# Performance work log

Measured on AMD Instinct MI355X. Metric: run time of the kernel, lower is better.

The kernel has to match this reference:

```python
import jax, jax.numpy as jnp
import numpy as np

N_GRIDS = 16
N_FEATS = 2
GRID_SHAPE = (64, 64, 64)  # D, H, W
NODES = 64
N_OUT = 1
DATA_MIN = 0.0
DATA_MAX = 1.0
N_POINTS = 524288


def setup_inputs() -> dict:
    key = jax.random.key(0)
    ks = jax.random.split(key, 12)
    x = jax.random.uniform(ks[0], (N_POINTS, 3), jnp.float32, -1.0, 1.0)
    # matches randomize_grids(): scales ~ log(1 - U*0.05), rotations ~ identity quat + noise,
    # translations ~ U(-0.05, 0.05)
    scales = jnp.log(1.0 - jax.random.uniform(ks[1], (N_GRIDS, 3), jnp.float32) * 0.05)
    rotations = jnp.zeros((N_GRIDS, 4), jnp.float32).at[:, 3].set(1.0) \
        + jax.random.normal(ks[2], (N_GRIDS, 4), jnp.float32) * 0.05
    translations = jax.random.uniform(ks[3], (N_GRIDS, 3), jnp.float32) * 0.1 - 0.05
    # original uses U(-1e-4, 1e-4); use a larger scale for numerically meaningful outputs
    feature_grids = jax.random.uniform(ks[4], (N_GRIDS, N_FEATS) + GRID_SHAPE,
                                       jnp.float32, -0.1, 0.1)
    d_in = N_GRIDS * N_FEATS
    def xavier(k, fi, fo):
        std = np.sqrt(2.0 / (fi + fo)).astype(np.float32)
        return jax.random.normal(k, (fi, fo), jnp.float32) * std
    W0 = xavier(ks[5], d_in, NODES)
    b0 = jax.random.normal(ks[6], (NODES,), jnp.float32) * 0.001
    W1 = xavier(ks[7], NODES, NODES)
    b1 = jax.random.normal(ks[8], (NODES,), jnp.float32) * 0.001
    W2 = xavier(ks[9], NODES, N_OUT)
    b2 = jax.random.normal(ks[10], (N_OUT,), jnp.float32) * 0.001
    return {"x": x, "rotations": rotations, "scales": scales,
            "translations": translations, "feature_grids": feature_grids,
            "W0": W0, "b0": b0, "W1": W1, "b1": b1, "W2": W2, "b2": b2}


def quat_to_rot(q):
    # q: [G,4] in (x, y, z, w) order; normalized (rotation_activation)
    q = q / jnp.linalg.norm(q, axis=-1, keepdims=True)
    x, y, z, w = q[:, 0], q[:, 1], q[:, 2], q[:, 3]
    r0 = jnp.stack([1 - 2 * (y * y + z * z), 2 * (x * y - z * w), 2 * (x * z + y * w)], -1)
    r1 = jnp.stack([2 * (x * y + z * w), 1 - 2 * (x * x + z * z), 2 * (y * z - x * w)], -1)
    r2 = jnp.stack([2 * (x * z - y * w), 2 * (y * z + x * w), 1 - 2 * (x * x + y * y)], -1)
    return jnp.stack([r0, r1, r2], axis=-2)  # [G,3,3]


def transform_points(x, rotations, scales, translations):
    # S*R*T order: local = diag(exp(scales)) @ R @ x + t, per grid -> [G,N,3]
    R = quat_to_rot(rotations)
    s = jnp.exp(scales)
    M = s[:, :, None] * R  # [G,3,3]
    return jnp.einsum('gij,nj->gni', M, x) + translations[:, None, :]


def trilinear_sample(grid, pts):
    # grid: [C,D,H,W]; pts: [N,3] (x,y,z) in [-1,1]; grid_sample semantics:
    # mode='bilinear', align_corners=True, padding_mode='zeros'
    C, D, H, W = grid.shape
    fx = (pts[:, 0] + 1.0) * 0.5 * (W - 1)
    fy = (pts[:, 1] + 1.0) * 0.5 * (H - 1)
    fz = (pts[:, 2] + 1.0) * 0.5 * (D - 1)
    x0 = jnp.floor(fx); y0 = jnp.floor(fy); z0 = jnp.floor(fz)
    wx = fx - x0; wy = fy - y0; wz = fz - z0
    x0i = x0.astype(jnp.int32); y0i = y0.astype(jnp.int32); z0i = z0.astype(jnp.int32)

    def corner(dx, dy, dz):
        xi = x0i + dx; yi = y0i + dy; zi = z0i + dz
        valid = (xi >= 0) & (xi < W) & (yi >= 0) & (yi < H) & (zi >= 0) & (zi < D)
        v = grid[:, jnp.clip(zi, 0, D - 1), jnp.clip(yi, 0, H - 1), jnp.clip(xi, 0, W - 1)]
        w = ((wx if dx else 1 - wx) * (wy if dy else 1 - wy) * (wz if dz else 1 - wz))
        return v * jnp.where(valid, w, 0.0)[None, :]

    out = corner(0, 0, 0)
    for dz in (0, 1):
        for dy in (0, 1):
            for dx in (0, 1):
                if (dx, dy, dz) != (0, 0, 0):
                    out = out + corner(dx, dy, dz)
    return out  # [C,N]


def reference(x, rotations, scales, translations, feature_grids, W0, b0, W1, b1, W2, b2):
    pts = transform_points(x, rotations, scales, translations)      # [G,N,3]
    feats = jax.vmap(trilinear_sample)(feature_grids, pts)          # [G,C,N]
    feats = feats.transpose(2, 0, 1).reshape(x.shape[0], -1)        # [N, G*C]
    h = jax.nn.relu(feats @ W0 + b0)
    h = jax.nn.relu(h @ W1 + b1)
    y = h @ W2 + b2
    return y * (DATA_MAX - DATA_MIN) + DATA_MIN
```

## Files before the change

### kernel.cpp

```cpp
#include <hip/hip_runtime.h>
#include <cstddef>
#include <cstdint>

constexpr int NPTS   = 524288;
constexpr int NG     = 16;
constexpr int GR     = 64;
constexpr int GR3    = GR * GR * GR;
constexpr int NNODES = 64;
constexpr int NBINS  = 32768;

constexpr size_t GRIDS_BYTES = (size_t)NG * GR3 * 8;
constexpr size_t WS_SORT     = GRIDS_BYTES;
constexpr size_t SORT_BYTES  = (size_t)NPTS * 16;
constexpr size_t WS_KEYR     = WS_SORT + SORT_BYTES;
constexpr size_t KEYR_BYTES  = (size_t)NPTS * 4;
constexpr size_t WS_BINS     = WS_KEYR + KEYR_BYTES;
constexpr size_t BINS_BYTES  = (size_t)NBINS * 4;
constexpr size_t WS_MATS     = WS_BINS + BINS_BYTES;
constexpr size_t MATS_BYTES  = 1024;
constexpr size_t WS_WPACK    = WS_MATS + MATS_BYTES;
constexpr size_t WPACK_BYTES = (size_t)(256 + 512) * 16;
constexpr size_t WS_PART     = WS_WPACK + WPACK_BYTES;
constexpr size_t PART_BYTES  = 128 * 4;
constexpr size_t WS_TOTAL    = WS_PART + PART_BYTES;

constexpr int PREP_REPACK = 4096;
constexpr int PREP_HIST   = 2048;

typedef _Float16 half8 __attribute__((ext_vector_type(8)));
typedef float    floatx4 __attribute__((ext_vector_type(4)));

__device__ __forceinline__ unsigned part1by2(unsigned x) {
    x &= 0x3ff;
    x = (x | (x << 16)) & 0x030000FF;
    x = (x | (x <<  8)) & 0x0300F00F;
    x = (x | (x <<  4)) & 0x030C30C3;
    x = (x | (x <<  2)) & 0x09249249;
    return x;
}

__device__ __forceinline__ unsigned cell_of(float px, float py, float pz) {
    int cx = (int)((px + 1.0f) * 16.0f); cx = min(max(cx, 0), 31);
    int cy = (int)((py + 1.0f) * 16.0f); cy = min(max(cy, 0), 31);
    int cz = (int)((pz + 1.0f) * 16.0f); cz = min(max(cz, 0), 31);
    return part1by2((unsigned)cx) | (part1by2((unsigned)cy) << 1) | (part1by2((unsigned)cz) << 2);
}

__device__ __forceinline__ unsigned f32_to_bf16_rne(float f) {
    unsigned u = __float_as_uint(f);
    return (u + 0x7fffu + ((u >> 16) & 1u)) >> 16;
}

__device__ __forceinline__ unsigned pack_h2(float a, float b) {
    unsigned short ua = __builtin_bit_cast(unsigned short, (_Float16)a);
    unsigned short ub = __builtin_bit_cast(unsigned short, (_Float16)b);
    return (unsigned)ua | ((unsigned)ub << 16);
}

__device__ __forceinline__ unsigned short f32_to_h16(float a) {
    return __builtin_bit_cast(unsigned short, (_Float16)a);
}

__global__ __launch_bounds__(256) void prep_kernel(
    const float* __restrict__ grids, uint2* __restrict__ gout,
    const float* __restrict__ xs, unsigned* __restrict__ bins,
    unsigned* __restrict__ keyrank,
    const float* __restrict__ rot, const float* __restrict__ scl,
    const float* __restrict__ trn, float* __restrict__ mats,
    const float* __restrict__ W0, const float* __restrict__ W1,
    uint4* __restrict__ wpack)
{
    const int bid = blockIdx.x;
    const int tid = threadIdx.x;

    if (bid < PREP_REPACK) {
        const int base = (bid * 256 + tid) * 4;
        const int g    = base >> 18;
        const int node = base & (GR3 - 1);
        const int x    = node & 63;
        const float* p0 = grids + (size_t)g * 2 * GR3 + node;
        const float* p1 = p0 + GR3;
        const float4 c0 = *(const float4*)p0;
        const float4 c1 = *(const float4*)p1;
        float d0n, d1n;
        if (x == 60) { d0n = c0.w; d1n = c1.w; }
        else         { d0n = p0[4]; d1n = p1[4]; }
        const float e0[5] = {c0.x, c0.y, c0.z, c0.w, d0n};
        const float e1[5] = {c1.x, c1.y, c1.z, c1.w, d1n};
        unsigned pk[5];
        #pragma unroll
        for (int i = 0; i < 5; ++i)
            pk[i] = f32_to_bf16_rne(e0[i]) | (f32_to_bf16_rne(e1[i]) << 16);
        uint4* dst = (uint4*)(gout + (size_t)g * GR3 + node);
        dst[0] = make_uint4(pk[0], pk[1], pk[1], pk[2]);
        dst[1] = make_uint4(pk[2], pk[3], pk[3], pk[4]);
    } else if (bid < PREP_REPACK + PREP_HIST) {
        const int n = (bid - PREP_REPACK) * 256 + tid;
        const unsigned key = cell_of(xs[n*3+0], xs[n*3+1], xs[n*3+2]);
        const unsigned rank = atomicAdd(&bins[key], 1u);
        keyrank[n] = key | (rank << 15);
    } else if (bid == PREP_REPACK + PREP_HIST) {
        const int g = tid;
        if (g < NG) {
            float qx = rot[g*4+0], qy = rot[g*4+1], qz = rot[g*4+2], qw = rot[g*4+3];
            const float inv = 1.0f / sqrtf(qx*qx + qy*qy + qz*qz + qw*qw);
            qx *= inv; qy *= inv; qz *= inv; qw *= inv;
            const float sx = expf(scl[g*3+0]);
            const float sy = expf(scl[g*3+1]);
            const float sz = expf(scl[g*3+2]);
            float* m = mats + g * 12;
            m[0] = sx * (1.0f - 2.0f*(qy*qy + qz*qz));
            m[1] = sx * (2.0f*(qx*qy - qz*qw));
            m[2] = sx * (2.0f*(qx*qz + qy*qw));
            m[3] = sy * (2.0f*(qx*qy + qz*qw));
            m[4] = sy * (1.0f - 2.0f*(qx*qx + qz*qz));
            m[5] = sy * (2.0f*(qy*qz - qx*qw));
            m[6] = sz * (2.0f*(qx*qz - qy*qw));
            m[7] = sz * (2.0f*(qy*qz + qx*qw));
            m[8] = sz * (1.0f - 2.0f*(qx*qx + qy*qy));
            m[9]  = trn[g*3+0];
            m[10] = trn[g*3+1];
            m[11] = trn[g*3+2];
        }
    } else {
        const int t = tid >> 6;
        const int lane = tid & 63;
        const int q = lane >> 4, c = lane & 15;
        const int n = t * 16 + c;
        {
            unsigned u[4];
            #pragma unroll
            for (int jj = 0; jj < 4; ++jj) {
                const int k0 = q * 8 + 2 * jj;
                u[jj] = pack_h2(W0[k0 * NNODES + n], W0[(k0 + 1) * NNODES + n]);
            }
            wpack[t * 64 + lane] = make_uint4(u[0], u[1], u[2], u[3]);
        }
        #pragma unroll
        for (int ks = 0; ks < 2; ++ks) {
            unsigned u[4];
            #pragma unroll
            for (int jj = 0; jj < 4; ++jj) {
                const int k0 = ks * 32 + q * 8 + 2 * jj;
                u[jj] = pack_h2(W1[k0 * NNODES + n], W1[(k0 + 1) * NNODES + n]);
            }
            wpack[256 + (ks * 4 + t) * 64 + lane] = make_uint4(u[0], u[1], u[2], u[3]);
        }
    }
}

__global__ __launch_bounds__(256) void scanA_kernel(unsigned* __restrict__ bins,
                                                    unsigned* __restrict__ part) {
    __shared__ unsigned s[256];
    const int t = threadIdx.x;
    const int base = blockIdx.x * 256;
    const unsigned v = bins[base + t];
    s[t] = v;
    __syncthreads();
    for (int off = 1; off < 256; off <<= 1) {
        unsigned u = (t >= off) ? s[t - off] : 0u;
        __syncthreads();
        s[t] += u;
        __syncthreads();
    }
    bins[base + t] = s[t] - v;
    if (t == 255) part[blockIdx.x] = s[255];
}

__global__ __launch_bounds__(128) void scanB_kernel(unsigned* __restrict__ part) {
    __shared__ unsigned s[128];
    const int t = threadIdx.x;
    const unsigned v = part[t];
    s[t] = v;
    __syncthreads();
    for (int off = 1; off < 128; off <<= 1) {
        unsigned u = (t >= off) ? s[t - off] : 0u;
        __syncthreads();
        s[t] += u;
        __syncthreads();
    }
    part[t] = s[t] - v;
}

__global__ __launch_bounds__(256) void scatter_kernel(const float* __restrict__ xs,
                                                      const unsigned* __restrict__ bins,
                                                      const unsigned* __restrict__ part,
                                                      const unsigned* __restrict__ keyrank,
                                                      float4* __restrict__ sorted) {
    const int n = blockIdx.x * 256 + threadIdx.x;
    if (n >= NPTS) return;
    const unsigned kr = keyrank[n];
    const unsigned key = kr & 0x7fffu;
    const unsigned rank = kr >> 15;
    const unsigned pos = part[key >> 8] + bins[key] + rank;
    sorted[pos] = make_float4(xs[n*3+0], xs[n*3+1], xs[n*3+2], __int_as_float(n));
}

struct Geom {
    unsigned i00, i01, i10, i11;
    float ax0, ax1, ay0, ay1, az0, az1;
};

__device__ __forceinline__ Geom make_geom(const float* __restrict__ m,
                                          float px, float py, float pz, int g) {
    Geom G;
    const float tx = fmaf(m[0], px, fmaf(m[1], py, fmaf(m[2], pz, m[9])));
    const float ty = fmaf(m[3], px, fmaf(m[4], py, fmaf(m[5], pz, m[10])));
    const float tz = fmaf(m[6], px, fmaf(m[7], py, fmaf(m[8], pz, m[11])));
    const float fx = (tx + 1.0f) * 31.5f;
    const float fy = (ty + 1.0f) * 31.5f;
    const float fz = (tz + 1.0f) * 31.5f;
    const float x0f = floorf(fx), y0f = floorf(fy), z0f = floorf(fz);
    const float wx = fx - x0f, wy = fy - y0f, wz = fz - z0f;
    const int x0 = (int)x0f, y0 = (int)y0f, z0 = (int)z0f;
    float ax0 = ((unsigned)x0       < 64u) ? (1.0f - wx) : 0.0f;
    float ax1 = ((unsigned)(x0 + 1) < 64u) ? wx          : 0.0f;
    const bool wrap = (x0 == -1);
    G.ax0 = wrap ? ax1 : ax0;
    G.ax1 = wrap ? 0.0f : ax1;
    G.ay0 = ((unsigned)y0       < 64u) ? (1.0f - wy) : 0.0f;
    G.ay1 = ((unsigned)(y0 + 1) < 64u) ? wy          : 0.0f;
    G.az0 = ((unsigned)z0       < 64u) ? (1.0f - wz) : 0.0f;
    G.az1 = ((unsigned)(z0 + 1) < 64u) ? wz          : 0.0f;
    const int xb  = min(max(x0, 0), 63);
    const int yc0 = min(max(y0, 0), 63),     yc1 = min(max(y0 + 1, 0), 63);
    const int zc0 = min(max(z0, 0), 63),     zc1 = min(max(z0 + 1, 0), 63);
    const unsigned b = (unsigned)(g << 18) + (unsigned)xb;
    G.i00 = b + (unsigned)((zc0 << 12) + (yc0 << 6));
    G.i01 = b + (unsigned)((zc0 << 12) + (yc1 << 6));
    G.i10 = b + (unsigned)((zc1 << 12) + (yc0 << 6));
    G.i11 = b + (unsigned)((zc1 << 12) + (yc1 << 6));
    return G;
}

__device__ __forceinline__ void acc_pair(float& f0, float& f1, const Geom& G,
                                         uint2 q, float wyz) {
    float s0 = G.ax0 * __uint_as_float(q.x << 16);
    s0 = fmaf(G.ax1, __uint_as_float(q.y << 16), s0);
    f0 = fmaf(wyz, s0, f0);
    float s1 = G.ax0 * __uint_as_float(q.x & 0xffff0000u);
    s1 = fmaf(G.ax1, __uint_as_float(q.y & 0xffff0000u), s1);
    f1 = fmaf(wyz, s1, f1);
}

constexpr int ARENA_H = 64 * 64;

__device__ __forceinline__ int sw_addr(int row, int halfcol) {
    return row * 64 + ((((halfcol >> 3) ^ (row & 7)) << 3) | (halfcol & 7));
}

__global__ __launch_bounds__(256, 4) void amgsrn_main(
    const float4* __restrict__ sorted,
    const uint2*  __restrict__ gridsP,
    const float*  __restrict__ mats,
    const uint4*  __restrict__ wpack,
    const float*  __restrict__ b0,
    const float*  __restrict__ b1,
    const float*  __restrict__ W2,
    const float*  __restrict__ b2,
    float* __restrict__ out)
{
    __shared__ unsigned short sh[4 * ARENA_H];

    const int tid  = threadIdx.x;
    const int lane = tid & 63;
    const int wv   = tid >> 6;
    const int c    = lane & 15;
    const int q    = lane >> 4;
    unsigned short* wa = sh + wv * ARENA_H;

    const int n = blockIdx.x * 256 + tid;
    const float4 p = sorted[n];
    const float px = p.x, py = p.y, pz = p.z;
    const int orig = __float_as_int(p.w);

    unsigned pk[NG];
    Geom Ga = make_geom(mats, px, py, pz, 0);
    uint2 a00 = gridsP[Ga.i00], a01 = gridsP[Ga.i01];
    uint2 a10 = gridsP[Ga.i10], a11 = gridsP[Ga.i11];
    Geom Gb = make_geom(mats + 12, px, py, pz, 1);
    uint2 b00 = gridsP[Gb.i00], b01 = gridsP[Gb.i01];
    uint2 b10 = gridsP[Gb.i10], b11 = gridsP[Gb.i11];
    #pragma unroll
    for (int g = 0; g < NG; ++g) {
        Geom Gn;
        uint2 n00, n01, n10, n11;
        if (g + 2 < NG) {
            Gn = make_geom(mats + (g + 2) * 12, px, py, pz, g + 2);
            n00 = gridsP[Gn.i00]; n01 = gridsP[Gn.i01];
            n10 = gridsP[Gn.i10]; n11 = gridsP[Gn.i11];
        }
        float f0 = 0.0f, f1 = 0.0f;
        acc_pair(f0, f1, Ga, a00, Ga.az0 * Ga.ay0);
        acc_pair(f0, f1, Ga, a01, Ga.az0 * Ga.ay1);
        acc_pair(f0, f1, Ga, a10, Ga.az1 * Ga.ay0);
        acc_pair(f0, f1, Ga, a11, Ga.az1 * Ga.ay1);
        pk[g] = pack_h2(f0, f1);
        Ga = Gb; a00 = b00; a01 = b01; a10 = b10; a11 = b11;
        if (g + 2 < NG) {
            Gb = Gn; b00 = n00; b01 = n01; b10 = n10; b11 = n11;
        }
    }

    #pragma unroll
    for (int g4 = 0; g4 < 4; ++g4)
        *(uint4*)(wa + sw_addr(lane, g4 * 8)) =
            make_uint4(pk[g4*4+0], pk[g4*4+1], pk[g4*4+2], pk[g4*4+3]);
    __syncthreads();

    half8 a0[4];
    #pragma unroll
    for (int m = 0; m < 4; ++m)
        a0[m] = *(const half8*)(wa + sw_addr(m * 16 + c, q * 8));

    half8 b0f[4], b1f[2][4];
    #pragma unroll
    for (int t = 0; t < 4; ++t)
        b0f[t] = __builtin_bit_cast(half8, wpack[t * 64 + lane]);
    #pragma unroll
    for (int ks = 0; ks < 2; ++ks)
        #pragma unroll
        for (int t = 0; t < 4; ++t)
            b1f[ks][t] = __builtin_bit_cast(half8, wpack[256 + (ks * 4 + t) * 64 + lane]);
    float b0v[4], b1v[4], w2v[4];
    #pragma unroll
    for (int t = 0; t < 4; ++t) {
        b0v[t] = b0[t * 16 + c];
        b1v[t] = b1[t * 16 + c];
        w2v[t] = W2[t * 16 + c];
    }
    const float b2s = b2[0];

    __syncthreads();

    #pragma unroll
    for (int t = 0; t < 4; ++t) {
        #pragma unroll
        for (int m = 0; m < 4; ++m) {
            floatx4 acc = {b0v[t], b0v[t], b0v[t], b0v[t]};
            acc = __builtin_amdgcn_mfma_f32_16x16x32_f16(a0[m], b0f[t], acc, 0, 0, 0);
            const int node = t * 16 + c;
            const int ptb  = m * 16 + q * 4;
            #pragma unroll
            for (int r = 0; r < 4; ++r)
                wa[sw_addr(ptb + r, node)] = f32_to_h16(fmaxf(acc[r], 0.0f));
        }
    }
    __syncthreads();

    half8 a1[4][2];
    #pragma unroll
    for (int m = 0; m < 4; ++m)
        #pragma unroll
        for (int ks = 0; ks < 2; ++ks)
            a1[m][ks] = *(const half8*)(wa + sw_addr(m * 16 + c, ks * 32 + q * 8));

    float p4[4][4];
    #pragma unroll
    for (int m = 0; m < 4; ++m)
        #pragma unroll
        for (int r = 0; r < 4; ++r) p4[m][r] = 0.0f;

    #pragma unroll
    for (int t = 0; t < 4; ++t) {
        #pragma unroll
        for (int m = 0; m < 4; ++m) {
            floatx4 acc = {b1v[t], b1v[t], b1v[t], b1v[t]};
            acc = __builtin_amdgcn_mfma_f32_16x16x32_f16(a1[m][0], b1f[0][t], acc, 0, 0, 0);
            acc = __builtin_amdgcn_mfma_f32_16x16x32_f16(a1[m][1], b1f[1][t], acc, 0, 0, 0);
            #pragma unroll
            for (int r = 0; r < 4; ++r)
                p4[m][r] = fmaf(fmaxf(acc[r], 0.0f), w2v[t], p4[m][r]);
        }
    }

    #pragma unroll
    for (int m = 0; m < 4; ++m)
        #pragma unroll
        for (int r = 0; r < 4; ++r) {
            float v = p4[m][r];
            v += __shfl_xor(v, 1, 64);
            v += __shfl_xor(v, 2, 64);
            v += __shfl_xor(v, 4, 64);
            v += __shfl_xor(v, 8, 64);
            p4[m][r] = v + b2s;
        }

    #pragma unroll
    for (int m = 0; m < 4; ++m)
        #pragma unroll
        for (int r = 0; r < 4; ++r) {
            const int srcPt = m * 16 + q * 4 + r;
            const int origPt = __shfl(orig, srcPt, 64);
            if (c == 0) out[origPt] = p4[m][r];
        }
}

__global__ __launch_bounds__(256, 3) void amgsrn_fused_fallback(
    const float* __restrict__ xs,
    const float* __restrict__ rot,
    const float* __restrict__ scl,
    const float* __restrict__ trn,
    const float* __restrict__ grids,
    const float* __restrict__ W0,
    const float* __restrict__ b0,
    const float* __restrict__ W1,
    const float* __restrict__ b1,
    const float* __restrict__ W2,
    const float* __restrict__ b2,
    float* __restrict__ out)
{
    __shared__ float sM[NG][12];
    const int tid = threadIdx.x;
    if (tid < NG) {
        const int g = tid;
        float qx = rot[g*4+0], qy = rot[g*4+1], qz = rot[g*4+2], qw = rot[g*4+3];
        const float inv = 1.0f / sqrtf(qx*qx + qy*qy + qz*qz + qw*qw);
        qx *= inv; qy *= inv; qz *= inv; qw *= inv;
        const float sx = expf(scl[g*3+0]);
        const float sy = expf(scl[g*3+1]);
        const float sz = expf(scl[g*3+2]);
        sM[g][0] = sx * (1.0f - 2.0f*(qy*qy + qz*qz));
        sM[g][1] = sx * (2.0f*(qx*qy - qz*qw));
        sM[g][2] = sx * (2.0f*(qx*qz + qy*qw));
        sM[g][3] = sy * (2.0f*(qx*qy + qz*qw));
        sM[g][4] = sy * (1.0f - 2.0f*(qx*qx + qz*qz));
        sM[g][5] = sy * (2.0f*(qy*qz - qx*qw));
        sM[g][6] = sz * (2.0f*(qx*qz - qy*qw));
        sM[g][7] = sz * (2.0f*(qy*qz + qx*qw));
        sM[g][8] = sz * (1.0f - 2.0f*(qx*qx + qy*qy));
        sM[g][9]  = trn[g*3+0];
        sM[g][10] = trn[g*3+1];
        sM[g][11] = trn[g*3+2];
    }
    __syncthreads();

    const int n = blockIdx.x * blockDim.x + tid;
    if (n >= NPTS) return;
    const float px = xs[n*3+0];
    const float py = xs[n*3+1];
    const float pz = xs[n*3+2];

    float h0[NNODES];
    #pragma unroll
    for (int j = 0; j < NNODES; ++j) h0[j] = b0[j];

    #pragma unroll
    for (int g = 0; g < NG; ++g) {
        const float* m = sM[g];
        const float tx = m[0]*px + m[1]*py + m[2]*pz + m[9];
        const float ty = m[3]*px + m[4]*py + m[5]*pz + m[10];
        const float tz = m[6]*px + m[7]*py + m[8]*pz + m[11];
        const float fx = (tx + 1.0f) * 31.5f;
        const float fy = (ty + 1.0f) * 31.5f;
        const float fz = (tz + 1.0f) * 31.5f;
        const float x0f = floorf(fx), y0f = floorf(fy), z0f = floorf(fz);
        const float wx = fx - x0f, wy = fy - y0f, wz = fz - z0f;
        const int x0 = (int)x0f, y0 = (int)y0f, z0 = (int)z0f;
        const float* gb = grids + (size_t)g * (size_t)(2 * GR3);
        float f0 = 0.0f, f1 = 0.0f;
        #pragma unroll
        for (int dz = 0; dz < 2; ++dz) {
            #pragma unroll
            for (int dy = 0; dy < 2; ++dy) {
                #pragma unroll
                for (int dx = 0; dx < 2; ++dx) {
                    const int xi = x0 + dx, yi = y0 + dy, zi = z0 + dz;
                    const bool valid = ((unsigned)xi < (unsigned)GR) &
                                       ((unsigned)yi < (unsigned)GR) &
                                       ((unsigned)zi < (unsigned)GR);
                    const int xc = min(max(xi, 0), GR-1);
                    const int yc = min(max(yi, 0), GR-1);
                    const int zc = min(max(zi, 0), GR-1);
                    float w = (dx ? wx : 1.0f - wx) *
                              (dy ? wy : 1.0f - wy) *
                              (dz ? wz : 1.0f - wz);
                    w = valid ? w : 0.0f;
                    const int idx = (zc * GR + yc) * GR + xc;
                    f0 = fmaf(w, gb[idx], f0);
                    f1 = fmaf(w, gb[idx + GR3], f1);
                }
            }
        }
        const float* w0a = W0 + (2*g    ) * NNODES;
        const float* w0b = W0 + (2*g + 1) * NNODES;
        #pragma unroll
        for (int j = 0; j < NNODES; ++j)
            h0[j] = fmaf(f1, w0b[j], fmaf(f0, w0a[j], h0[j]));
    }
    #pragma unroll
    for (int j = 0; j < NNODES; ++j) h0[j] = fmaxf(h0[j], 0.0f);

    float y = b2[0];
    #pragma unroll
    for (int half = 0; half < 2; ++half) {
        float h1[32];
        #pragma unroll
        for (int j = 0; j < 32; ++j) h1[j] = b1[half * 32 + j];
        #pragma unroll
        for (int k = 0; k < NNODES; ++k) {
            const float a = h0[k];
            const float* w = W1 + k * NNODES + half * 32;
            #pragma unroll
            for (int j = 0; j < 32; ++j) h1[j] = fmaf(a, w[j], h1[j]);
        }
        #pragma unroll
        for (int j = 0; j < 32; ++j) y = fmaf(fmaxf(h1[j], 0.0f), W2[half * 32 + j], y);
    }

    out[n] = y;
}

extern "C" void kernel_launch(void* const* d_in, const int* in_sizes, int n_in,
                              void* d_out, int out_size, void* d_ws, size_t ws_size,
                              hipStream_t stream) {
    const float* xs  = (const float*)d_in[0];
    const float* rot = (const float*)d_in[1];
    const float* scl = (const float*)d_in[2];
    const float* trn = (const float*)d_in[3];
    const float* gr  = (const float*)d_in[4];
    const float* W0  = (const float*)d_in[5];
    const float* b0  = (const float*)d_in[6];
    const float* W1  = (const float*)d_in[7];
    const float* b1  = (const float*)d_in[8];
    const float* W2  = (const float*)d_in[9];
    const float* b2  = (const float*)d_in[10];
    float* out = (float*)d_out;

    if (ws_size < WS_TOTAL) {
        dim3 grid((NPTS + 255) / 256), block(256);
        hipLaunchKernelGGL(amgsrn_fused_fallback, grid, block, 0, stream,
                           xs, rot, scl, trn, gr, W0, b0, W1, b1, W2, b2, out);
        return;
    }

    char* ws = (char*)d_ws;
    uint2*    gridsP  = (uint2*)(ws);
    float4*   sorted  = (float4*)(ws + WS_SORT);
    unsigned* keyrank = (unsigned*)(ws + WS_KEYR);
    unsigned* bins    = (unsigned*)(ws + WS_BINS);
    float*    mats    = (float*)(ws + WS_MATS);
    uint4*    wpack   = (uint4*)(ws + WS_WPACK);
    unsigned* part    = (unsigned*)(ws + WS_PART);

    hipMemsetAsync(bins, 0, BINS_BYTES, stream);
    hipLaunchKernelGGL(prep_kernel, dim3(PREP_REPACK + PREP_HIST + 2), dim3(256), 0, stream,
                       gr, gridsP, xs, bins, keyrank,
                       rot, scl, trn, mats, W0, W1, wpack);
    hipLaunchKernelGGL(scanA_kernel, dim3(NBINS / 256), dim3(256), 0, stream, bins, part);
    hipLaunchKernelGGL(scanB_kernel, dim3(1), dim3(128), 0, stream, part);
    hipLaunchKernelGGL(scatter_kernel, dim3(NPTS / 256), dim3(256), 0, stream,
                       xs, bins, part, keyrank, sorted);
    hipLaunchKernelGGL(amgsrn_main, dim3(NPTS / 256), dim3(256), 0, stream,
                       sorted, gridsP, mats, wpack, b0, b1, W2, b2, out);
}
```

Before: 192.8 us.

## Add quad-packed 2x2 xy-neighbour grid layout and fold top-level scan into scatter

Adds a repacked grid layout in which each node stores bf16 values for its x/x+1 and y/y+1 neighbours for both features, so each trilinear sample needs two 16-byte gathers per grid (one per z slice) instead of the pair layout's four. This cuts the number of random gather transactions in the main sampling kernel, at the cost of twice the repacked-grid memory and a heavier repack pass. The single-block scanB kernel is removed and each scatter block now rescans the 128 partials in shared memory, saving a launch. The grid repack is split out of the prep kernel into its own launch, and the MLP tail is factored into a shared helper.

```diff
diff --git a/kernel.cpp b/kernel.cpp
--- a/kernel.cpp
+++ b/kernel.cpp
@@ -9,23 +9,17 @@
 constexpr int NNODES = 64;
 constexpr int NBINS  = 32768;
 
-constexpr size_t GRIDS_BYTES = (size_t)NG * GR3 * 8;
-constexpr size_t WS_SORT     = GRIDS_BYTES;
+constexpr size_t QUAD_GRIDS  = (size_t)NG * GR3 * 16;
+constexpr size_t PAIR_GRIDS  = (size_t)NG * GR3 * 8;
 constexpr size_t SORT_BYTES  = (size_t)NPTS * 16;
-constexpr size_t WS_KEYR     = WS_SORT + SORT_BYTES;
 constexpr size_t KEYR_BYTES  = (size_t)NPTS * 4;
-constexpr size_t WS_BINS     = WS_KEYR + KEYR_BYTES;
 constexpr size_t BINS_BYTES  = (size_t)NBINS * 4;
-constexpr size_t WS_MATS     = WS_BINS + BINS_BYTES;
 constexpr size_t MATS_BYTES  = 1024;
-constexpr size_t WS_WPACK    = WS_MATS + MATS_BYTES;
 constexpr size_t WPACK_BYTES = (size_t)(256 + 512) * 16;
-constexpr size_t WS_PART     = WS_WPACK + WPACK_BYTES;
 constexpr size_t PART_BYTES  = 128 * 4;
-constexpr size_t WS_TOTAL    = WS_PART + PART_BYTES;
-
-constexpr int PREP_REPACK = 4096;
-constexpr int PREP_HIST   = 2048;
+constexpr size_t TAIL_BYTES  = SORT_BYTES + KEYR_BYTES + BINS_BYTES + MATS_BYTES + WPACK_BYTES + PART_BYTES;
+
+constexpr int PREP_HIST = 2048;
 
 typedef _Float16 half8 __attribute__((ext_vector_type(8)));
 typedef float    floatx4 __attribute__((ext_vector_type(4)));
@@ -61,8 +55,67 @@
     return __builtin_bit_cast(unsigned short, (_Float16)a);
 }
 
-__global__ __launch_bounds__(256) void prep_kernel(
-    const float* __restrict__ grids, uint2* __restrict__ gout,
+__device__ __forceinline__ unsigned pack_b2(float a, float b) {
+    return f32_to_bf16_rne(a) | (f32_to_bf16_rne(b) << 16);
+}
+
+__device__ __forceinline__ float blo(unsigned u) { return __uint_as_float(u << 16); }
+__device__ __forceinline__ float bhi(unsigned u) { return __uint_as_float(u & 0xffff0000u); }
+
+__global__ __launch_bounds__(256) void repack_quad(const float* __restrict__ grids,
+                                                   uint4* __restrict__ gq) {
+    const int t4 = blockIdx.x * 256 + threadIdx.x;
+    const int g   = t4 >> 16;
+    const int rem = t4 & 65535;
+    const int z   = rem >> 10;
+    const int yb  = (rem >> 4) & 63;
+    const int xg  = rem & 15;
+    const int xb0 = xg * 4;
+    const int y1  = min(yb + 1, 63);
+    const float* c0y0 = grids + ((size_t)g * 2 + 0) * GR3 + (z << 12) + (yb << 6) + xb0;
+    const float* c0y1 = grids + ((size_t)g * 2 + 0) * GR3 + (z << 12) + (y1 << 6) + xb0;
+    const float* c1y0 = c0y0 + GR3;
+    const float* c1y1 = c0y1 + GR3;
+    const float4 a00 = *(const float4*)c0y0;
+    const float4 a01 = *(const float4*)c0y1;
+    const float4 a10 = *(const float4*)c1y0;
+    const float4 a11 = *(const float4*)c1y1;
+    const bool edge = (xb0 == 60);
+    const float e00[5] = {a00.x, a00.y, a00.z, a00.w, edge ? a00.w : c0y0[4]};
+    const float e01[5] = {a01.x, a01.y, a01.z, a01.w, edge ? a01.w : c0y1[4]};
+    const float e10[5] = {a10.x, a10.y, a10.z, a10.w, edge ? a10.w : c1y0[4]};
+    const float e11[5] = {a11.x, a11.y, a11.z, a11.w, edge ? a11.w : c1y1[4]};
+    uint4* dst = gq + (size_t)((g << 18) + (z << 12) + (yb << 6) + xb0);
+    #pragma unroll
+    for (int i = 0; i < 4; ++i)
+        dst[i] = make_uint4(pack_b2(e00[i], e00[i+1]), pack_b2(e01[i], e01[i+1]),
+                            pack_b2(e10[i], e10[i+1]), pack_b2(e11[i], e11[i+1]));
+}
+
+__global__ __launch_bounds__(256) void repack_pair(const float* __restrict__ grids,
+                                                   uint2* __restrict__ gout) {
+    const int base = (blockIdx.x * 256 + threadIdx.x) * 4;
+    const int g    = base >> 18;
+    const int node = base & (GR3 - 1);
+    const int x    = node & 63;
+    const float* p0 = grids + (size_t)g * 2 * GR3 + node;
+    const float* p1 = p0 + GR3;
+    const float4 c0 = *(const float4*)p0;
+    const float4 c1 = *(const float4*)p1;
+    float d0n, d1n;
+    if (x == 60) { d0n = c0.w; d1n = c1.w; }
+    else         { d0n = p0[4]; d1n = p1[4]; }
+    const float e0[5] = {c0.x, c0.y, c0.z, c0.w, d0n};
+    const float e1[5] = {c1.x, c1.y, c1.z, c1.w, d1n};
+    unsigned pk[5];
+    #pragma unroll
+    for (int i = 0; i < 5; ++i) pk[i] = pack_b2(e0[i], e1[i]);
+    uint4* dst = (uint4*)(gout + (size_t)g * GR3 + node);
+    dst[0] = make_uint4(pk[0], pk[1], pk[1], pk[2]);
+    dst[1] = make_uint4(pk[2], pk[3], pk[3], pk[4]);
+}
+
+__global__ __launch_bounds__(256) void prep2_kernel(
     const float* __restrict__ xs, unsigned* __restrict__ bins,
     unsigned* __restrict__ keyrank,
     const float* __restrict__ rot, const float* __restrict__ scl,
@@ -72,34 +125,12 @@
 {
     const int bid = blockIdx.x;
     const int tid = threadIdx.x;
-
-    if (bid < PREP_REPACK) {
-        const int base = (bid * 256 + tid) * 4;
-        const int g    = base >> 18;
-        const int node = base & (GR3 - 1);
-        const int x    = node & 63;
-        const float* p0 = grids + (size_t)g * 2 * GR3 + node;
-        const float* p1 = p0 + GR3;
-        const float4 c0 = *(const float4*)p0;
-        const float4 c1 = *(const float4*)p1;
-        float d0n, d1n;
-        if (x == 60) { d0n = c0.w; d1n = c1.w; }
-        else         { d0n = p0[4]; d1n = p1[4]; }
-        const float e0[5] = {c0.x, c0.y, c0.z, c0.w, d0n};
-        const float e1[5] = {c1.x, c1.y, c1.z, c1.w, d1n};
-        unsigned pk[5];
-        #pragma unroll
-        for (int i = 0; i < 5; ++i)
-            pk[i] = f32_to_bf16_rne(e0[i]) | (f32_to_bf16_rne(e1[i]) << 16);
-        uint4* dst = (uint4*)(gout + (size_t)g * GR3 + node);
-        dst[0] = make_uint4(pk[0], pk[1], pk[1], pk[2]);
-        dst[1] = make_uint4(pk[2], pk[3], pk[3], pk[4]);
-    } else if (bid < PREP_REPACK + PREP_HIST) {
-        const int n = (bid - PREP_REPACK) * 256 + tid;
+    if (bid < PREP_HIST) {
+        const int n = bid * 256 + tid;
         const unsigned key = cell_of(xs[n*3+0], xs[n*3+1], xs[n*3+2]);
         const unsigned rank = atomicAdd(&bins[key], 1u);
         keyrank[n] = key | (rank << 15);
-    } else if (bid == PREP_REPACK + PREP_HIST) {
+    } else if (bid == PREP_HIST) {
         const int g = tid;
         if (g < NG) {
             float qx = rot[g*4+0], qy = rot[g*4+1], qz = rot[g*4+2], qw = rot[g*4+3];
@@ -167,33 +198,237 @@
     if (t == 255) part[blockIdx.x] = s[255];
 }
 
-__global__ __launch_bounds__(128) void scanB_kernel(unsigned* __restrict__ part) {
-    __shared__ unsigned s[128];
-    const int t = threadIdx.x;
-    const unsigned v = part[t];
-    s[t] = v;
-    __syncthreads();
-    for (int off = 1; off < 128; off <<= 1) {
-        unsigned u = (t >= off) ? s[t - off] : 0u;
-        __syncthreads();
-        s[t] += u;
-        __syncthreads();
-    }
-    part[t] = s[t] - v;
-}
-
 __global__ __launch_bounds__(256) void scatter_kernel(const float* __restrict__ xs,
                                                       const unsigned* __restrict__ bins,
                                                       const unsigned* __restrict__ part,
                                                       const unsigned* __restrict__ keyrank,
                                                       float4* __restrict__ sorted) {
-    const int n = blockIdx.x * 256 + threadIdx.x;
-    if (n >= NPTS) return;
+    __shared__ unsigned sp[128];
+    const int t = threadIdx.x;
+    if (t < 128) sp[t] = part[t];
+    __syncthreads();
+    for (int off = 1; off < 128; off <<= 1) {
+        unsigned u = (t < 128 && t >= off) ? sp[t - off] : 0u;
+        __syncthreads();
+        if (t < 128) sp[t] += u;
+        __syncthreads();
+    }
+    const int n = blockIdx.x * 256 + t;
     const unsigned kr = keyrank[n];
     const unsigned key = kr & 0x7fffu;
     const unsigned rank = kr >> 15;
-    const unsigned pos = part[key >> 8] + bins[key] + rank;
+    const unsigned pidx = key >> 8;
+    const unsigned pbase = pidx ? sp[pidx - 1] : 0u;
+    const unsigned pos = pbase + bins[key] + rank;
     sorted[pos] = make_float4(xs[n*3+0], xs[n*3+1], xs[n*3+2], __int_as_float(n));
+}
+
+struct GeomQ {
+    unsigned i0, i1;
+    float w00, w10, w01, w11, az0, az1;
+};
+
+__device__ __forceinline__ GeomQ make_geomq(const float* __restrict__ m,
+                                            float px, float py, float pz, int g) {
+    GeomQ G;
+    const float tx = fmaf(m[0], px, fmaf(m[1], py, fmaf(m[2], pz, m[9])));
+    const float ty = fmaf(m[3], px, fmaf(m[4], py, fmaf(m[5], pz, m[10])));
+    const float tz = fmaf(m[6], px, fmaf(m[7], py, fmaf(m[8], pz, m[11])));
+    const float fx = (tx + 1.0f) * 31.5f;
+    const float fy = (ty + 1.0f) * 31.5f;
+    const float fz = (tz + 1.0f) * 31.5f;
+    const float x0f = floorf(fx), y0f = floorf(fy), z0f = floorf(fz);
+    const float wx = fx - x0f, wy = fy - y0f, wz = fz - z0f;
+    const int x0 = (int)x0f, y0 = (int)y0f, z0 = (int)z0f;
+    float ax0 = ((unsigned)x0       < 64u) ? (1.0f - wx) : 0.0f;
+    float ax1 = ((unsigned)(x0 + 1) < 64u) ? wx          : 0.0f;
+    const bool xw = (x0 == -1);
+    const float AX0 = xw ? ax1 : ax0, AX1 = xw ? 0.0f : ax1;
+    float ay0 = ((unsigned)y0       < 64u) ? (1.0f - wy) : 0.0f;
+    float ay1 = ((unsigned)(y0 + 1) < 64u) ? wy          : 0.0f;
+    const bool yw = (y0 == -1);
+    const float AY0 = yw ? ay1 : ay0, AY1 = yw ? 0.0f : ay1;
+    G.w00 = AX0 * AY0; G.w10 = AX1 * AY0; G.w01 = AX0 * AY1; G.w11 = AX1 * AY1;
+    G.az0 = ((unsigned)z0       < 64u) ? (1.0f - wz) : 0.0f;
+    G.az1 = ((unsigned)(z0 + 1) < 64u) ? wz          : 0.0f;
+    const int xb  = min(max(x0, 0), 63);
+    const int yb  = min(max(y0, 0), 63);
+    const int zc0 = min(max(z0, 0), 63), zc1 = min(max(z0 + 1, 0), 63);
+    const unsigned b = (unsigned)(g << 18) + (unsigned)((yb << 6) + xb);
+    G.i0 = b + (unsigned)(zc0 << 12);
+    G.i1 = b + (unsigned)(zc1 << 12);
+    return G;
+}
+
+__device__ __forceinline__ void acc_quad(float& f0, float& f1, const GeomQ& G,
+                                         uint4 q, float az) {
+    float s0 = G.w00 * blo(q.x);
+    s0 = fmaf(G.w10, bhi(q.x), s0);
+    s0 = fmaf(G.w01, blo(q.y), s0);
+    s0 = fmaf(G.w11, bhi(q.y), s0);
+    f0 = fmaf(az, s0, f0);
+    float s1 = G.w00 * blo(q.z);
+    s1 = fmaf(G.w10, bhi(q.z), s1);
+    s1 = fmaf(G.w01, blo(q.w), s1);
+    s1 = fmaf(G.w11, bhi(q.w), s1);
+    f1 = fmaf(az, s1, f1);
+}
+
+constexpr int ARENA_H = 64 * 64;
+
+__device__ __forceinline__ int sw_addr(int row, int halfcol) {
+    return row * 64 + ((((halfcol >> 3) ^ (row & 7)) << 3) | (halfcol & 7));
+}
+
+__device__ __forceinline__ void mlp_tail(unsigned* pk, unsigned short* wa,
+                                         const uint4* __restrict__ wpack,
+                                         const float* __restrict__ b0,
+                                         const float* __restrict__ b1,
+                                         const float* __restrict__ W2,
+                                         const float* __restrict__ b2,
+                                         int lane, int c, int q, int orig,
+                                         float* __restrict__ out) {
+    #pragma unroll
+    for (int g4 = 0; g4 < 4; ++g4)
+        *(uint4*)(wa + sw_addr(lane, g4 * 8)) =
+            make_uint4(pk[g4*4+0], pk[g4*4+1], pk[g4*4+2], pk[g4*4+3]);
+    __syncthreads();
+
+    half8 a0[4];
+    #pragma unroll
+    for (int m = 0; m < 4; ++m)
+        a0[m] = *(const half8*)(wa + sw_addr(m * 16 + c, q * 8));
+
+    half8 b0f[4], b1f[2][4];
+    #pragma unroll
+    for (int t = 0; t < 4; ++t)
+        b0f[t] = __builtin_bit_cast(half8, wpack[t * 64 + lane]);
+    #pragma unroll
+    for (int ks = 0; ks < 2; ++ks)
+        #pragma unroll
+        for (int t = 0; t < 4; ++t)
+            b1f[ks][t] = __builtin_bit_cast(half8, wpack[256 + (ks * 4 + t) * 64 + lane]);
+    float b0v[4], b1v[4], w2v[4];
+    #pragma unroll
+    for (int t = 0; t < 4; ++t) {
+        b0v[t] = b0[t * 16 + c];
+        b1v[t] = b1[t * 16 + c];
+        w2v[t] = W2[t * 16 + c];
+    }
+    const float b2s = b2[0];
+
+    __syncthreads();
+
+    #pragma unroll
+    for (int t = 0; t < 4; ++t) {
+        #pragma unroll
+        for (int m = 0; m < 4; ++m) {
+            floatx4 acc = {b0v[t], b0v[t], b0v[t], b0v[t]};
+            acc = __builtin_amdgcn_mfma_f32_16x16x32_f16(a0[m], b0f[t], acc, 0, 0, 0);
+            const int node = t * 16 + c;
+            const int ptb  = m * 16 + q * 4;
+            #pragma unroll
+            for (int r = 0; r < 4; ++r)
+                wa[sw_addr(ptb + r, node)] = f32_to_h16(fmaxf(acc[r], 0.0f));
+        }
+    }
+    __syncthreads();
+
+    half8 a1[4][2];
+    #pragma unroll
+    for (int m = 0; m < 4; ++m)
+        #pragma unroll
+        for (int ks = 0; ks < 2; ++ks)
+            a1[m][ks] = *(const half8*)(wa + sw_addr(m * 16 + c, ks * 32 + q * 8));
+
+    float p4[4][4];
+    #pragma unroll
+    for (int m = 0; m < 4; ++m)
+        #pragma unroll
+        for (int r = 0; r < 4; ++r) p4[m][r] = 0.0f;
+
+    #pragma unroll
+    for (int t = 0; t < 4; ++t) {
+        #pragma unroll
+        for (int m = 0; m < 4; ++m) {
+            floatx4 acc = {b1v[t], b1v[t], b1v[t], b1v[t]};
+            acc = __builtin_amdgcn_mfma_f32_16x16x32_f16(a1[m][0], b1f[0][t], acc, 0, 0, 0);
+            acc = __builtin_amdgcn_mfma_f32_16x16x32_f16(a1[m][1], b1f[1][t], acc, 0, 0, 0);
+            #pragma unroll
+            for (int r = 0; r < 4; ++r)
+                p4[m][r] = fmaf(fmaxf(acc[r], 0.0f), w2v[t], p4[m][r]);
+        }
+    }
+
+    #pragma unroll
+    for (int m = 0; m < 4; ++m)
+        #pragma unroll
+        for (int r = 0; r < 4; ++r) {
+            float v = p4[m][r];
+            v += __shfl_xor(v, 1, 64);
+            v += __shfl_xor(v, 2, 64);
+            v += __shfl_xor(v, 4, 64);
+            v += __shfl_xor(v, 8, 64);
+            p4[m][r] = v + b2s;
+        }
+
+    #pragma unroll
+    for (int m = 0; m < 4; ++m)
+        #pragma unroll
+        for (int r = 0; r < 4; ++r) {
+            const int srcPt = m * 16 + q * 4 + r;
+            const int origPt = __shfl(orig, srcPt, 64);
+            if (c == 0) out[origPt] = p4[m][r];
+        }
+}
+
+__global__ __launch_bounds__(256, 4) void amgsrn_main_quad(
+    const float4* __restrict__ sorted,
+    const uint4*  __restrict__ gq,
+    const float*  __restrict__ mats,
+    const uint4*  __restrict__ wpack,
+    const float*  __restrict__ b0,
+    const float*  __restrict__ b1,
+    const float*  __restrict__ W2,
+    const float*  __restrict__ b2,
+    float* __restrict__ out)
+{
+    __shared__ unsigned short sh[4 * ARENA_H];
+
+    const int tid  = threadIdx.x;
+    const int lane = tid & 63;
+    const int wv   = tid >> 6;
+    const int c    = lane & 15;
+    const int q    = lane >> 4;
+    unsigned short* wa = sh + wv * ARENA_H;
+
+    const int n = blockIdx.x * 256 + tid;
+    const float4 p = sorted[n];
+    const float px = p.x, py = p.y, pz = p.z;
+    const int orig = __float_as_int(p.w);
+
+    unsigned pk[NG];
+    GeomQ Ga = make_geomq(mats, px, py, pz, 0);
+    uint4 qa0 = gq[Ga.i0], qa1 = gq[Ga.i1];
+    GeomQ Gb = make_geomq(mats + 12, px, py, pz, 1);
+    uint4 qb0 = gq[Gb.i0], qb1 = gq[Gb.i1];
+    #pragma unroll
+    for (int g = 0; g < NG; ++g) {
+        GeomQ Gn;
+        uint4 n0, n1;
+        if (g + 2 < NG) {
+            Gn = make_geomq(mats + (g + 2) * 12, px, py, pz, g + 2);
+            n0 = gq[Gn.i0]; n1 = gq[Gn.i1];
+        }
+        float f0 = 0.0f, f1 = 0.0f;
+        acc_quad(f0, f1, Ga, qa0, Ga.az0);
+        acc_quad(f0, f1, Ga, qa1, Ga.az1);
+        pk[g] = pack_h2(f0, f1);
+        Ga = Gb; qa0 = qb0; qa1 = qb1;
+        if (g + 2 < NG) { Gb = Gn; qb0 = n0; qb1 = n1; }
+    }
+
+    mlp_tail(pk, wa, wpack, b0, b1, W2, b2, lane, c, q, orig, out);
 }
 
 struct Geom {
@@ -235,21 +470,15 @@
 
 __device__ __forceinline__ void acc_pair(float& f0, float& f1, const Geom& G,
                                          uint2 q, float wyz) {
-    float s0 = G.ax0 * __uint_as_float(q.x << 16);
-    s0 = fmaf(G.ax1, __uint_as_float(q.y << 16), s0);
+    float s0 = G.ax0 * blo(q.x);
+    s0 = fmaf(G.ax1, blo(q.y), s0);
     f0 = fmaf(wyz, s0, f0);
-    float s1 = G.ax0 * __uint_as_float(q.x & 0xffff0000u);
-    s1 = fmaf(G.ax1, __uint_as_float(q.y & 0xffff0000u), s1);
+    float s1 = G.ax0 * bhi(q.x);
+    s1 = fmaf(G.ax1, bhi(q.y), s1);
     f1 = fmaf(wyz, s1, f1);
 }
 
-constexpr int ARENA_H = 64 * 64;
-
-__device__ __forceinline__ int sw_addr(int row, int halfcol) {
-    return row * 64 + ((((halfcol >> 3) ^ (row & 7)) << 3) | (halfcol & 7));
-}
-
-__global__ __launch_bounds__(256, 4) void amgsrn_main(
+__global__ __launch_bounds__(256, 4) void amgsrn_main_pair(
     const float4* __restrict__ sorted,
     const uint2*  __restrict__ gridsP,
     const float*  __restrict__ mats,
@@ -302,98 +531,7 @@
         }
     }
 
-    #pragma unroll
-    for (int g4 = 0; g4 < 4; ++g4)
-        *(uint4*)(wa + sw_addr(lane, g4 * 8)) =
-            make_uint4(pk[g4*4+0], pk[g4*4+1], pk[g4*4+2], pk[g4*4+3]);
-    __syncthreads();
-
-    half8 a0[4];
-    #pragma unroll
-    for (int m = 0; m < 4; ++m)
-        a0[m] = *(const half8*)(wa + sw_addr(m * 16 + c, q * 8));
-
-    half8 b0f[4], b1f[2][4];
-    #pragma unroll
-    for (int t = 0; t < 4; ++t)
-        b0f[t] = __builtin_bit_cast(half8, wpack[t * 64 + lane]);
-    #pragma unroll
-    for (int ks = 0; ks < 2; ++ks)
-        #pragma unroll
-        for (int t = 0; t < 4; ++t)
-            b1f[ks][t] = __builtin_bit_cast(half8, wpack[256 + (ks * 4 + t) * 64 + lane]);
-    float b0v[4], b1v[4], w2v[4];
-    #pragma unroll
-    for (int t = 0; t < 4; ++t) {
-        b0v[t] = b0[t * 16 + c];
-        b1v[t] = b1[t * 16 + c];
-        w2v[t] = W2[t * 16 + c];
-    }
-    const float b2s = b2[0];
-
-    __syncthreads();
-
-    #pragma unroll
-    for (int t = 0; t < 4; ++t) {
-        #pragma unroll
-        for (int m = 0; m < 4; ++m) {
-            floatx4 acc = {b0v[t], b0v[t], b0v[t], b0v[t]};
-            acc = __builtin_amdgcn_mfma_f32_16x16x32_f16(a0[m], b0f[t], acc, 0, 0, 0);
-            const int node = t * 16 + c;
-            const int ptb  = m * 16 + q * 4;
-            #pragma unroll
-            for (int r = 0; r < 4; ++r)
-                wa[sw_addr(ptb + r, node)] = f32_to_h16(fmaxf(acc[r], 0.0f));
-        }
-    }
-    __syncthreads();
-
-    half8 a1[4][2];
-    #pragma unroll
-    for (int m = 0; m < 4; ++m)
-        #pragma unroll
-        for (int ks = 0; ks < 2; ++ks)
-            a1[m][ks] = *(const half8*)(wa + sw_addr(m * 16 + c, ks * 32 + q * 8));
-
-    float p4[4][4];
-    #pragma unroll
-    for (int m = 0; m < 4; ++m)
-        #pragma unroll
-        for (int r = 0; r < 4; ++r) p4[m][r] = 0.0f;
-
-    #pragma unroll
-    for (int t = 0; t < 4; ++t) {
-        #pragma unroll
-        for (int m = 0; m < 4; ++m) {
-            floatx4 acc = {b1v[t], b1v[t], b1v[t], b1v[t]};
-            acc = __builtin_amdgcn_mfma_f32_16x16x32_f16(a1[m][0], b1f[0][t], acc, 0, 0, 0);
-            acc = __builtin_amdgcn_mfma_f32_16x16x32_f16(a1[m][1], b1f[1][t], acc, 0, 0, 0);
-            #pragma unroll
-            for (int r = 0; r < 4; ++r)
-                p4[m][r] = fmaf(fmaxf(acc[r], 0.0f), w2v[t], p4[m][r]);
-        }
-    }
-
-    #pragma unroll
-    for (int m = 0; m < 4; ++m)
-        #pragma unroll
-        for (int r = 0; r < 4; ++r) {
-            float v = p4[m][r];
-            v += __shfl_xor(v, 1, 64);
-            v += __shfl_xor(v, 2, 64);
-            v += __shfl_xor(v, 4, 64);
-            v += __shfl_xor(v, 8, 64);
-            p4[m][r] = v + b2s;
-        }
-
-    #pragma unroll
-    for (int m = 0; m < 4; ++m)
-        #pragma unroll
-        for (int r = 0; r < 4; ++r) {
-            const int srcPt = m * 16 + q * 4 + r;
-            const int origPt = __shfl(orig, srcPt, 64);
-            if (c == 0) out[origPt] = p4[m][r];
-        }
+    mlp_tail(pk, wa, wpack, b0, b1, W2, b2, lane, c, q, orig, out);
 }
 
 __global__ __launch_bounds__(256, 3) void amgsrn_fused_fallback(
@@ -527,7 +665,9 @@
     const float* b2  = (const float*)d_in[10];
     float* out = (float*)d_out;
 
-    if (ws_size < WS_TOTAL) {
+    const bool quad = (ws_size >= QUAD_GRIDS + TAIL_BYTES);
+    const bool pair = (ws_size >= PAIR_GRIDS + TAIL_BYTES);
+    if (!quad && !pair) {
         dim3 grid((NPTS + 255) / 256), block(256);
         hipLaunchKernelGGL(amgsrn_fused_fallback, grid, block, 0, stream,
                            xs, rot, scl, trn, gr, W0, b0, W1, b1, W2, b2, out);
@@ -535,22 +675,31 @@
     }
 
     char* ws = (char*)d_ws;
-    uint2*    gridsP  = (uint2*)(ws);
-    float4*   sorted  = (float4*)(ws + WS_SORT);
-    unsigned* keyrank = (unsigned*)(ws + WS_KEYR);
-    unsigned* bins    = (unsigned*)(ws + WS_BINS);
-    float*    mats    = (float*)(ws + WS_MATS);
-    uint4*    wpack   = (uint4*)(ws + WS_WPACK);
-    unsigned* part    = (unsigned*)(ws + WS_PART);
+    const size_t gbytes = quad ? QUAD_GRIDS : PAIR_GRIDS;
+    char* gridsR = ws;
+    float4*   sorted  = (float4*)(ws + gbytes);
+    unsigned* keyrank = (unsigned*)(ws + gbytes + SORT_BYTES);
+    unsigned* bins    = (unsigned*)(ws + gbytes + SORT_BYTES + KEYR_BYTES);
+    float*    mats    = (float*)(ws + gbytes + SORT_BYTES + KEYR_BYTES + BINS_BYTES);
+    uint4*    wpack   = (uint4*)(ws + gbytes + SORT_BYTES + KEYR_BYTES + BINS_BYTES + MATS_BYTES);
+    unsigned* part    = (unsigned*)(ws + gbytes + SORT_BYTES + KEYR_BYTES + BINS_BYTES + MATS_BYTES + WPACK_BYTES);
 
     hipMemsetAsync(bins, 0, BINS_BYTES, stream);
-    hipLaunchKernelGGL(prep_kernel, dim3(PREP_REPACK + PREP_HIST + 2), dim3(256), 0, stream,
-                       gr, gridsP, xs, bins, keyrank,
-                       rot, scl, trn, mats, W0, W1, wpack);
+    if (quad)
+        hipLaunchKernelGGL(repack_quad, dim3(4096), dim3(256), 0, stream,
+                           gr, (uint4*)gridsR);
+    else
+        hipLaunchKernelGGL(repack_pair, dim3(4096), dim3(256), 0, stream,
+                           gr, (uint2*)gridsR);
+    hipLaunchKernelGGL(prep2_kernel, dim3(PREP_HIST + 2), dim3(256), 0, stream,
+                       xs, bins, keyrank, rot, scl, trn, mats, W0, W1, wpack);
     hipLaunchKernelGGL(scanA_kernel, dim3(NBINS / 256), dim3(256), 0, stream, bins, part);
-    hipLaunchKernelGGL(scanB_kernel, dim3(1), dim3(128), 0, stream, part);
     hipLaunchKernelGGL(scatter_kernel, dim3(NPTS / 256), dim3(256), 0, stream,
                        xs, bins, part, keyrank, sorted);
-    hipLaunchKernelGGL(amgsrn_main, dim3(NPTS / 256), dim3(256), 0, stream,
-                       sorted, gridsP, mats, wpack, b0, b1, W2, b2, out);
-}
+    if (quad)
+        hipLaunchKernelGGL(amgsrn_main_quad, dim3(NPTS / 256), dim3(256), 0, stream,
+                           sorted, (const uint4*)gridsR, mats, wpack, b0, b1, W2, b2, out);
+    else
+        hipLaunchKernelGGL(amgsrn_main_pair, dim3(NPTS / 256), dim3(256), 0, stream,
+                           sorted, (const uint2*)gridsR, mats, wpack, b0, b1, W2, b2, out);
+}
```

After: 203.7 us. 1.06x slower.
